# Optimization experiments

Measured on AMD Instinct MI355X. Metric: run time of the kernel, lower is better.

## Reference

```python
import jax, jax.numpy as jnp
import numpy as np

N_NODES = 50000
HIDDEN = 256
DEPTH = 6
NUM_GRAPHS = 500


def _build_graph(n):
    # 4-regular directed graph: node i -> (i+1, i-1, i+5, i-5) mod n.
    offs = np.array([1, -1, 5, -5], dtype=np.int64)
    src = np.repeat(np.arange(n, dtype=np.int64), 4)
    dst = (src + np.tile(offs, n)) % n
    # incoming edge ids of node u (edge id = 4*src + offset_index)
    u = np.arange(n, dtype=np.int64)
    incoming = np.stack([4 * ((u - 1) % n) + 0,
                         4 * ((u + 1) % n) + 1,
                         4 * ((u - 5) % n) + 2,
                         4 * ((u + 5) % n) + 3], axis=1)  # [n,4]
    E = 4 * n
    pred = incoming[src]           # [E,4] candidate line-graph predecessors of edge e
    pred_src = pred // 4           # source node of each predecessor edge
    keep = pred_src != dst[:, None]  # drop backtracking edge (exactly 1 per row)
    lg_src = pred[keep]                                   # [3E]
    lg_dst = np.repeat(np.arange(E, dtype=np.int64), 4)[keep.ravel()]  # [3E]
    return src, dst, lg_src, lg_dst


def setup_inputs() -> dict:
    key = jax.random.key(0)
    ks = jax.random.split(key, 8)
    n, H = N_NODES, HIDDEN
    E = 4 * n
    _, dst, lg_src, lg_dst = _build_graph(n)
    graph_ids = np.arange(n, dtype=np.int64) // (n // NUM_GRAPHS)
    s = 0.02  # small weight scale keeps relu message passing stable over DEPTH iters
    return {
        "x_nodes": jax.random.normal(ks[0], (n, 35), jnp.float32),
        "x_edges": jax.random.normal(ks[1], (E, 40), jnp.float32),
        "t_m": jax.random.normal(ks[2], (E, H), jnp.float32) * 0.1,
        "W_i": jax.random.normal(ks[3], (40, H), jnp.float32) * s,
        "W_h": jax.random.normal(ks[4], (H, H), jnp.float32) * s,
        "W_o": jax.random.normal(ks[5], (35 + H, H), jnp.float32) * s,
        "b_o": jax.random.normal(ks[6], (H,), jnp.float32) * s,
        "edge_dst": jnp.asarray(dst, jnp.int32),
        "lg_src": jnp.asarray(lg_src, jnp.int32),
        "lg_dst": jnp.asarray(lg_dst, jnp.int32),
        "graph_ids": jnp.asarray(graph_ids, jnp.int32),
        "num_graphs": NUM_GRAPHS,
    }


def reference(x_nodes, x_edges, t_m, W_i, W_h, W_o, b_o,
              edge_dst, lg_src, lg_dst, graph_ids, num_graphs):
    E = x_edges.shape[0]
    n = x_nodes.shape[0]
    binput = x_edges @ W_i                       # W_i has no bias
    g_m = jax.nn.relu(binput)                    # [E,H] per-edge message
    # tree-message aggregation over line graph is constant across depth iters
    t_agg = jax.ops.segment_sum(t_m[lg_src], lg_dst, num_segments=E)
    for _ in range(DEPTH - 1):
        g_agg = jax.ops.segment_sum(g_m[lg_src], lg_dst, num_segments=E)
        g_m = jax.nn.relu(binput + (g_agg + t_agg) @ W_h)
    # edge -> dst-node aggregation (copy_e + sum)
    nei1 = jax.ops.segment_sum(g_m, edge_dst, num_segments=n)
    nei2 = jax.ops.segment_sum(t_m, edge_dst, num_segments=n)
    ainput = jnp.concatenate([x_nodes, nei1 + nei2], axis=1)  # [n, 35+H]
    atom_hiddens = jax.nn.relu(ainput @ W_o + b_o)
    # dgl.mean_nodes: per-graph mean of node features
    sums = jax.ops.segment_sum(atom_hiddens, graph_ids, num_segments=num_graphs)
    counts = jax.ops.segment_sum(jnp.ones((n, 1), atom_hiddens.dtype), graph_ids,
                                 num_segments=num_graphs)
    return sums / counts
```

## Files before the change

kernel.cpp:

```cpp
#include <hip/hip_runtime.h>


#define H 256

typedef __attribute__((ext_vector_type(4))) float f32x4;
typedef __attribute__((ext_vector_type(8))) short bf16x8;

#define MFMA(a, b, c) __builtin_amdgcn_mfma_f32_16x16x32_bf16((a), (b), (c), 0, 0, 0)

__device__ __forceinline__ float bf2f(ushort u) {
  union { unsigned int i; float f; } v; v.i = ((unsigned int)u) << 16; return v.f;
}
__device__ __forceinline__ ushort f2bf(float f) {
  union { float f; unsigned int i; } v; v.f = f;
  unsigned int i = v.i;
  i += 0x7fffu + ((i >> 16) & 1u);
  return (ushort)(i >> 16);
}

union AFrag { bf16x8 v; ushort u[8]; };

__device__ __forceinline__ int edge_delta(int o) {
  return ((o & 2) ? 5 : 1) * ((o & 1) ? -1 : 1);
}

__device__ __forceinline__ int phi(int L) {
  return (L & ~31) | (((L >> 2) & 1) << 4) | (((L >> 3) & 3) << 2) | (L & 3);
}

__global__ __launch_bounds__(256) void prep_weights_kernel(
    const float* __restrict__ Wh, const float* __restrict__ Wi, const float* __restrict__ Wo,
    ushort* __restrict__ WhF, ushort* __restrict__ WiT,
    ushort* __restrict__ WoT1, ushort* __restrict__ WoT2) {
  const int nn = blockIdx.x;
  const int t = threadIdx.x;
  const int w = phi(nn);
  const int ch = w >> 7, nf = (w >> 4) & 7, l15 = w & 15;
  const int ks = t >> 5, kg = (t >> 3) & 3, i = t & 7;
  WhF[ch * 32768 + ((nf * 8 + ks) << 9) + (kg * 16 + l15) * 8 + i] = f2bf(Wh[t * H + nn]);
  WoT2[nn * H + t] = f2bf(Wo[(35 + t) * H + nn]);
  if (t < 64) {
    WiT[w * 64 + t] = (t < 40) ? f2bf(Wi[t * H + nn]) : (ushort)0;
    WoT1[nn * 64 + t] = (t < 35) ? f2bf(Wo[t * H + nn]) : (ushort)0;
  }
}

__global__ __launch_bounds__(256) void sum_tm_kernel(
    const float* __restrict__ t_m, ushort* __restrict__ t3, ushort* __restrict__ t4,
    int n, int useT4) {
  const int idx = blockIdx.x * 256 + threadIdx.x;
  const int s = idx >> 5;
  if (s >= n) return;
  const int cg = (idx & 31) * 8;
  int im1 = s - 1; if (im1 < 0) im1 += n;
  int ip1 = s + 1; if (ip1 >= n) ip1 -= n;
  int im5 = s - 5; if (im5 < 0) im5 += n;
  int ip5 = s + 5; if (ip5 >= n) ip5 -= n;
  const size_t e0 = (size_t)(4 * im1 + 0) * H + cg;
  const size_t e1 = (size_t)(4 * ip1 + 1) * H + cg;
  const size_t e2 = (size_t)(4 * im5 + 2) * H + cg;
  const size_t e3 = (size_t)(4 * ip5 + 3) * H + cg;
  f32x4 v0a = *(const f32x4*)(t_m + e0), v0b = *(const f32x4*)(t_m + e0 + 4);
  f32x4 v1a = *(const f32x4*)(t_m + e1), v1b = *(const f32x4*)(t_m + e1 + 4);
  f32x4 v2a = *(const f32x4*)(t_m + e2), v2b = *(const f32x4*)(t_m + e2 + 4);
  f32x4 v3a = *(const f32x4*)(t_m + e3), v3b = *(const f32x4*)(t_m + e3 + 4);
  f32x4 Sa = v0a + v1a + v2a + v3a;
  f32x4 Sb = v0b + v1b + v2b + v3b;
  f32x4 ra[4] = {Sa - v1a, Sa - v0a, Sa - v3a, Sa - v2a};
  f32x4 rb[4] = {Sb - v1b, Sb - v0b, Sb - v3b, Sb - v2b};
#pragma unroll
  for (int o = 0; o < 4; ++o) {
    AFrag a;
#pragma unroll
    for (int i = 0; i < 4; ++i) { a.u[i] = f2bf(ra[o][i]); a.u[4 + i] = f2bf(rb[o][i]); }
    *(bf16x8*)(t3 + (size_t)(4 * s + o) * H + cg) = a.v;
  }
  if (useT4) {
    AFrag a;
#pragma unroll
    for (int i = 0; i < 4; ++i) { a.u[i] = f2bf(Sa[i]); a.u[4 + i] = f2bf(Sb[i]); }
    *(bf16x8*)(t4 + (size_t)s * H + cg) = a.v;
  }
}

__global__ __launch_bounds__(512, 4) void prologue_kernel(
    const float* __restrict__ x_edges, const ushort* __restrict__ t3,
    const ushort* __restrict__ WhF, const ushort* __restrict__ WiT,
    ushort* __restrict__ tb, ushort* __restrict__ g0P, int E, int n) {
  extern __shared__ ushort lds[];
  const int tid = threadIdx.x;
  const int wid = tid >> 6, lane = tid & 63, l15 = lane & 15, kg = lane >> 4;
  const int ch = blockIdx.x >> 9;
  const int colbase = ch << 7;

  {
    const bf16x8* src = (const bf16x8*)(WhF + (size_t)colbase * H);
    bf16x8* dstl = (bf16x8*)lds;
#pragma unroll
    for (int j = 0; j < 8; ++j) dstl[tid + j * 512] = src[tid + j * 512];
  }
  __syncthreads();

  const int nchunks = (E + 127) >> 7;
  for (int c = blockIdx.x & 511; c < nchunks; c += 512) {
    const int row0 = (c << 7) + wid * 16;
    if (row0 >= E) continue;
    const int r = row0 + l15;

    const float* xp = x_edges + (size_t)r * 40;
    f32x4 xa0 = *(const f32x4*)(xp + kg * 8);
    f32x4 xa1 = *(const f32x4*)(xp + kg * 8 + 4);
    f32x4 xb0, xb1;
    if (kg == 0) { xb0 = *(const f32x4*)(xp + 32); xb1 = *(const f32x4*)(xp + 36); }

    bf16x8 av[8];
#pragma unroll
    for (int ks = 0; ks < 8; ++ks)
      av[ks] = *(const bf16x8*)(t3 + (size_t)r * H + ks * 32 + kg * 8);

    f32x4 acc[8];
#pragma unroll
    for (int i = 0; i < 8; ++i) acc[i] = (f32x4){0.f, 0.f, 0.f, 0.f};

    AFrag bx0, bx1;
#pragma unroll
    for (int i = 0; i < 4; ++i) { bx0.u[i] = f2bf(xa0[i]); bx0.u[4 + i] = f2bf(xa1[i]); }
    if (kg == 0) {
#pragma unroll
      for (int i = 0; i < 4; ++i) { bx1.u[i] = f2bf(xb0[i]); bx1.u[4 + i] = f2bf(xb1[i]); }
    } else {
#pragma unroll
      for (int i = 0; i < 8; ++i) bx1.u[i] = 0;
    }
#pragma unroll
    for (int nf = 0; nf < 8; ++nf) {
      const int w = colbase + nf * 16 + l15;
      bf16x8 a0 = *(const bf16x8*)(WiT + w * 64 + kg * 8);
      acc[nf] = MFMA(a0, bx0.v, acc[nf]);
      bf16x8 a1 = *(const bf16x8*)(WiT + w * 64 + 32 + kg * 8);
      acc[nf] = MFMA(a1, bx1.v, acc[nf]);
    }

    const int s_ = r >> 2, o_ = r & 3;
    int d_ = s_ + edge_delta(o_);
    if (d_ < 0) d_ += n; else if (d_ >= n) d_ -= n;
    ushort* gout = g0P + (size_t)(4 * d_ + o_) * H + colbase + kg * 8;
#pragma unroll
    for (int tt = 0; tt < 4; ++tt) {
      AFrag pk;
#pragma unroll
      for (int i = 0; i < 4; ++i) {
        pk.u[i]     = f2bf(fmaxf(acc[2 * tt][i], 0.f));
        pk.u[4 + i] = f2bf(fmaxf(acc[2 * tt + 1][i], 0.f));
      }
      *(bf16x8*)(gout + tt * 32) = pk.v;
    }

#pragma unroll
    for (int ks = 0; ks < 8; ++ks) {
#pragma unroll
      for (int nf = 0; nf < 8; ++nf) {
        bf16x8 a = *(const bf16x8*)(lds + ((nf * 8 + ks) << 9) + (lane << 3));
        acc[nf] = MFMA(a, av[ks], acc[nf]);
      }
    }

    ushort* tbp = tb + (size_t)r * H + colbase + kg * 8;
#pragma unroll
    for (int tt = 0; tt < 4; ++tt) {
      AFrag pk;
#pragma unroll
      for (int i = 0; i < 4; ++i) {
        pk.u[i]     = f2bf(acc[2 * tt][i]);
        pk.u[4 + i] = f2bf(acc[2 * tt + 1][i]);
      }
      *(bf16x8*)(tbp + tt * 32) = pk.v;
    }
  }
}

__global__ __launch_bounds__(512, 4) void mp_iter_kernel(
    const ushort* __restrict__ gOldP, const ushort* __restrict__ tb,
    const ushort* __restrict__ WhF, ushort* __restrict__ gNewP, int E, int n) {
  extern __shared__ ushort lds[];
  const int tid = threadIdx.x;
  const int wid = tid >> 6, lane = tid & 63, l15 = lane & 15, kg = lane >> 4;
  const int ch = blockIdx.x >> 9;
  const int colbase = ch << 7;

  {
    const bf16x8* src = (const bf16x8*)(WhF + (size_t)colbase * H);
    bf16x8* dstl = (bf16x8*)lds;
#pragma unroll
    for (int j = 0; j < 8; ++j) dstl[tid + j * 512] = src[tid + j * 512];
  }
  __syncthreads();

  const int nchunks = (E + 127) >> 7;
  for (int c = blockIdx.x & 511; c < nchunks; c += 512) {
    const int row0 = (c << 7) + wid * 16;
    if (row0 >= E) continue;
    const int r = row0 + l15;

    bf16x8 av[8];
#pragma unroll
    for (int ks = 0; ks < 8; ++ks)
      av[ks] = *(const bf16x8*)(gOldP + (size_t)r * H + ks * 32 + kg * 8);

    bf16x8 tbv[4];
    const ushort* tbp = tb + (size_t)r * H + colbase + kg * 8;
#pragma unroll
    for (int tt = 0; tt < 4; ++tt) tbv[tt] = *(const bf16x8*)(tbp + tt * 32);

    f32x4 acc[8];
#pragma unroll
    for (int i = 0; i < 8; ++i) acc[i] = (f32x4){0.f, 0.f, 0.f, 0.f};

#pragma unroll
    for (int ks = 0; ks < 8; ++ks) {
#pragma unroll
      for (int nf = 0; nf < 8; ++nf) {
        bf16x8 a = *(const bf16x8*)(lds + ((nf * 8 + ks) << 9) + (lane << 3));
        acc[nf] = MFMA(a, av[ks], acc[nf]);
      }
    }

    const int s = r >> 2, o = r & 3;
    int d = s + edge_delta(o);
    if (d < 0) d += n; else if (d >= n) d -= n;
    ushort* gout = gNewP + (size_t)(4 * d + o) * H + colbase + kg * 8;
#pragma unroll
    for (int tt = 0; tt < 4; ++tt) {
      AFrag pk;
#pragma unroll
      for (int i = 0; i < 4; ++i) {
        const float G0 = acc[2 * tt][i];
        const float G1 = acc[2 * tt + 1][i];
        const float t0 = G0 + __shfl_xor(G0, 2);
        const float S0 = t0 + __shfl_xor(t0, 1);
        const float t1 = G1 + __shfl_xor(G1, 2);
        const float S1 = t1 + __shfl_xor(t1, 1);
        const float d0 = __shfl_xor(G0, 1);
        const float d1 = __shfl_xor(G1, 1);
        const float v0 = bf2f((ushort)tbv[tt][i])     + (S0 - d0);
        const float v1 = bf2f((ushort)tbv[tt][4 + i]) + (S1 - d1);
        pk.u[i]     = f2bf(fmaxf(v0, 0.f));
        pk.u[4 + i] = f2bf(fmaxf(v1, 0.f));
      }
      *(bf16x8*)(gout + tt * 32) = pk.v;
    }
  }
}

__global__ __launch_bounds__(256) void readout_kernel(
    const float* __restrict__ x_nodes, const float* __restrict__ t_m,
    const ushort* __restrict__ gP, const ushort* __restrict__ t4,
    const float* __restrict__ b_o,
    const ushort* __restrict__ WoT1, const ushort* __restrict__ WoT2,
    float* __restrict__ out, int n, int npg, int useT4) {
  const int gidx = blockIdx.x;
  const int wid = threadIdx.x >> 6;
  const int lane = threadIdx.x & 63;
  const int l15 = lane & 15;
  const int kg = lane >> 4;
  const int u0 = gidx * npg;

  __shared__ float red[H];

  f32x4 acc[2][16];
#pragma unroll
  for (int m = 0; m < 2; ++m)
#pragma unroll
    for (int i = 0; i < 16; ++i) acc[m][i] = (f32x4){0.f, 0.f, 0.f, 0.f};

  int uu[2]; bool mv[2]; int inc[2][4];
#pragma unroll
  for (int m = 0; m < 2; ++m) {
    const int mf = wid * 2 + m;
    const int rl = mf * 16 + l15;
    mv[m] = rl < npg;
    const int u = u0 + rl;
    uu[m] = u;
    if (mv[m]) {
      inc[m][0] = 4 * ((u - 1 + n) % n);
      inc[m][1] = 4 * ((u + 1) % n) + 1;
      inc[m][2] = 4 * ((u - 5 + n) % n) + 2;
      inc[m][3] = 4 * ((u + 5) % n) + 3;
    } else {
      inc[m][0] = inc[m][1] = inc[m][2] = inc[m][3] = 0;
    }
  }

#pragma unroll
  for (int ks = 0; ks < 2; ++ks) {
    const int k = ks * 32 + kg * 8;
#pragma unroll
    for (int m = 0; m < 2; ++m) {
      AFrag a;
#pragma unroll
      for (int i = 0; i < 8; ++i) {
        const int kk = k + i;
        a.u[i] = (mv[m] && kk < 35) ? f2bf(x_nodes[(size_t)uu[m] * 35 + kk]) : (ushort)0;
      }
#pragma unroll
      for (int nf = 0; nf < 16; ++nf) {
        bf16x8 b = *(const bf16x8*)(WoT1 + (nf * 16 + l15) * 64 + k);
        acc[m][nf] = MFMA(a.v, b, acc[m][nf]);
      }
    }
  }

#pragma unroll
  for (int ks = 0; ks < 8; ++ks) {
    const int k = ks * 32 + kg * 8;
#pragma unroll
    for (int m = 0; m < 2; ++m) {
      AFrag a;
      if (mv[m]) {
        float s[8];
#pragma unroll
        for (int i = 0; i < 8; ++i) s[i] = 0.f;
        const int e4 = 4 * uu[m];
#pragma unroll
        for (int j = 0; j < 4; ++j) {
          bf16x8 gv = *(const bf16x8*)(gP + (size_t)(e4 + j) * H + k);
#pragma unroll
          for (int i = 0; i < 8; ++i) s[i] += bf2f((ushort)gv[i]);
        }
        if (useT4) {
          bf16x8 tv = *(const bf16x8*)(t4 + (size_t)uu[m] * H + k);
#pragma unroll
          for (int i = 0; i < 8; ++i) s[i] += bf2f((ushort)tv[i]);
        } else {
#pragma unroll
          for (int j = 0; j < 4; ++j) {
            const float* tp = t_m + (size_t)inc[m][j] * H + k;
            f32x4 t0 = *(const f32x4*)tp;
            f32x4 t1 = *(const f32x4*)(tp + 4);
#pragma unroll
            for (int i = 0; i < 4; ++i) { s[i] += t0[i]; s[4 + i] += t1[i]; }
          }
        }
#pragma unroll
        for (int i = 0; i < 8; ++i) a.u[i] = f2bf(s[i]);
      } else {
#pragma unroll
        for (int i = 0; i < 8; ++i) a.u[i] = 0;
      }
#pragma unroll
      for (int nf = 0; nf < 16; ++nf) {
        bf16x8 b = *(const bf16x8*)(WoT2 + (nf * 16 + l15) * H + k);
        acc[m][nf] = MFMA(a.v, b, acc[m][nf]);
      }
    }
  }

  red[threadIdx.x] = 0.f;
  __syncthreads();

#pragma unroll
  for (int nf = 0; nf < 16; ++nf) {
    const int col = nf * 16 + l15;
    const float bias = b_o[col];
    float cs = 0.f;
#pragma unroll
    for (int m = 0; m < 2; ++m) {
#pragma unroll
      for (int j = 0; j < 4; ++j) {
        const int rr = (wid * 2 + m) * 16 + kg * 4 + j;
        if (rr < npg) cs += fmaxf(acc[m][nf][j] + bias, 0.f);
      }
    }
    cs += __shfl_xor(cs, 16);
    cs += __shfl_xor(cs, 32);
    if (kg == 0) atomicAdd(&red[col], cs);
  }
  __syncthreads();
  out[(size_t)gidx * H + threadIdx.x] = red[threadIdx.x] * (1.0f / (float)npg);
}

extern "C" void kernel_launch(void* const* d_in, const int* in_sizes, int n_in,
                              void* d_out, int out_size, void* d_ws, size_t ws_size,
                              hipStream_t stream) {
  const float* x_nodes = (const float*)d_in[0];
  const float* x_edges = (const float*)d_in[1];
  const float* t_m     = (const float*)d_in[2];
  const float* W_i     = (const float*)d_in[3];
  const float* W_h     = (const float*)d_in[4];
  const float* W_o     = (const float*)d_in[5];
  const float* b_o     = (const float*)d_in[6];
  (void)n_in;

  const int n = in_sizes[0] / 35;
  const int E = in_sizes[1] / 40;
  const int num_graphs = out_size / H;
  const int npg = n / num_graphs;

  char* ws = (char*)d_ws;
  ushort* WhF  = (ushort*)(ws);
  ushort* WiT  = (ushort*)(ws + 131072);
  ushort* WoT1 = (ushort*)(ws + 164 * 1024);
  ushort* WoT2 = (ushort*)(ws + 200 * 1024);
  size_t off = 336 * 1024;
  const size_t gbytes = (size_t)E * H * 2;
  ushort* tb = (ushort*)(ws + off); off += gbytes;
  ushort* gA = (ushort*)(ws + off); off += gbytes;
  ushort* gB = (ushort*)(ws + off); off += gbytes;
  ushort* t3 = gB;
  const size_t t4bytes = (size_t)n * H * 2;
  const int useT4 = (ws_size >= off + t4bytes) ? 1 : 0;
  ushort* t4 = (ushort*)(ws + off);

  prep_weights_kernel<<<256, 256, 0, stream>>>(W_h, W_i, W_o, WhF, WiT, WoT1, WoT2);
  sum_tm_kernel<<<(n * 32 + 255) / 256, 256, 0, stream>>>(t_m, t3, t4, n, useT4);
  prologue_kernel<<<1024, 512, 65536, stream>>>(x_edges, t3, WhF, WiT, tb, gA, E, n);

  ushort* src = gA;
  ushort* dst = gB;
  for (int it = 0; it < 5; ++it) {
    mp_iter_kernel<<<1024, 512, 65536, stream>>>(src, tb, WhF, dst, E, n);
    ushort* tmp = src; src = dst; dst = tmp;
  }

  readout_kernel<<<num_graphs, 256, 0, stream>>>(x_nodes, t_m, src, t4, b_o, WoT1, WoT2,
                                                 (float*)d_out, n, npg, useT4);
}
```

Before: 706.1 us.

## Split output columns into four 64-wide chunks to halve LDS and registers per block

The prologue and message-passing kernels now cover 64 output columns per block instead of 128, using 2048 blocks and 32 KB of LDS with launch bounds raised to 8 blocks per CU. The weight prep layout is reindexed so each 64-column chunk is contiguous. The A-operand rows are streamed with a two-deep rolling prefetch rather than all eight fragments held in registers, cutting register pressure to raise occupancy. In exchange, every input row of g and t3 is read by four blocks instead of two, doubling global and L2 read traffic for the A operand.

After: 890.3 us. 26.1% more time.

```diff
diff --git a/kernel.cpp b/kernel.cpp
--- a/kernel.cpp
+++ b/kernel.cpp
@@ -35,9 +35,9 @@
   const int nn = blockIdx.x;
   const int t = threadIdx.x;
   const int w = phi(nn);
-  const int ch = w >> 7, nf = (w >> 4) & 7, l15 = w & 15;
+  const int nfg = w >> 4, l15w = w & 15;
   const int ks = t >> 5, kg = (t >> 3) & 3, i = t & 7;
-  WhF[ch * 32768 + ((nf * 8 + ks) << 9) + (kg * 16 + l15) * 8 + i] = f2bf(Wh[t * H + nn]);
+  WhF[((nfg * 8 + ks) << 9) + ((kg << 4) + l15w) * 8 + i] = f2bf(Wh[t * H + nn]);
   WoT2[nn * H + t] = f2bf(Wo[(35 + t) * H + nn]);
   if (t < 64) {
     WiT[w * 64 + t] = (t < 40) ? f2bf(Wi[t * H + nn]) : (ushort)0;
@@ -83,7 +83,7 @@
   }
 }
 
-__global__ __launch_bounds__(512, 4) void prologue_kernel(
+__global__ __launch_bounds__(512, 8) void prologue_kernel(
     const float* __restrict__ x_edges, const ushort* __restrict__ t3,
     const ushort* __restrict__ WhF, const ushort* __restrict__ WiT,
     ushort* __restrict__ tb, ushort* __restrict__ g0P, int E, int n) {
@@ -91,13 +91,13 @@
   const int tid = threadIdx.x;
   const int wid = tid >> 6, lane = tid & 63, l15 = lane & 15, kg = lane >> 4;
   const int ch = blockIdx.x >> 9;
-  const int colbase = ch << 7;
+  const int colbase = ch << 6;
 
   {
-    const bf16x8* src = (const bf16x8*)(WhF + (size_t)colbase * H);
+    const bf16x8* src = (const bf16x8*)(WhF) + ch * 2048;
     bf16x8* dstl = (bf16x8*)lds;
 #pragma unroll
-    for (int j = 0; j < 8; ++j) dstl[tid + j * 512] = src[tid + j * 512];
+    for (int j = 0; j < 4; ++j) dstl[tid + j * 512] = src[tid + j * 512];
   }
   __syncthreads();
 
@@ -112,15 +112,13 @@
     f32x4 xa1 = *(const f32x4*)(xp + kg * 8 + 4);
     f32x4 xb0, xb1;
     if (kg == 0) { xb0 = *(const f32x4*)(xp + 32); xb1 = *(const f32x4*)(xp + 36); }
-
-    bf16x8 av[8];
-#pragma unroll
-    for (int ks = 0; ks < 8; ++ks)
-      av[ks] = *(const bf16x8*)(t3 + (size_t)r * H + ks * 32 + kg * 8);
-
-    f32x4 acc[8];
-#pragma unroll
-    for (int i = 0; i < 8; ++i) acc[i] = (f32x4){0.f, 0.f, 0.f, 0.f};
+    const ushort* t3r = t3 + (size_t)r * H + kg * 8;
+    bf16x8 av0 = *(const bf16x8*)(t3r);
+    bf16x8 av1 = *(const bf16x8*)(t3r + 32);
+
+    f32x4 acc[4];
+#pragma unroll
+    for (int i = 0; i < 4; ++i) acc[i] = (f32x4){0.f, 0.f, 0.f, 0.f};
 
     AFrag bx0, bx1;
 #pragma unroll
@@ -133,7 +131,7 @@
       for (int i = 0; i < 8; ++i) bx1.u[i] = 0;
     }
 #pragma unroll
-    for (int nf = 0; nf < 8; ++nf) {
+    for (int nf = 0; nf < 4; ++nf) {
       const int w = colbase + nf * 16 + l15;
       bf16x8 a0 = *(const bf16x8*)(WiT + w * 64 + kg * 8);
       acc[nf] = MFMA(a0, bx0.v, acc[nf]);
@@ -146,7 +144,7 @@
     if (d_ < 0) d_ += n; else if (d_ >= n) d_ -= n;
     ushort* gout = g0P + (size_t)(4 * d_ + o_) * H + colbase + kg * 8;
 #pragma unroll
-    for (int tt = 0; tt < 4; ++tt) {
+    for (int tt = 0; tt < 2; ++tt) {
       AFrag pk;
 #pragma unroll
       for (int i = 0; i < 4; ++i) {
@@ -158,16 +156,19 @@
 
 #pragma unroll
     for (int ks = 0; ks < 8; ++ks) {
-#pragma unroll
-      for (int nf = 0; nf < 8; ++nf) {
+      bf16x8 av2;
+      if (ks < 6) av2 = *(const bf16x8*)(t3r + (ks + 2) * 32);
+#pragma unroll
+      for (int nf = 0; nf < 4; ++nf) {
         bf16x8 a = *(const bf16x8*)(lds + ((nf * 8 + ks) << 9) + (lane << 3));
-        acc[nf] = MFMA(a, av[ks], acc[nf]);
-      }
+        acc[nf] = MFMA(a, av0, acc[nf]);
+      }
+      av0 = av1; av1 = av2;
     }
 
     ushort* tbp = tb + (size_t)r * H + colbase + kg * 8;
 #pragma unroll
-    for (int tt = 0; tt < 4; ++tt) {
+    for (int tt = 0; tt < 2; ++tt) {
       AFrag pk;
 #pragma unroll
       for (int i = 0; i < 4; ++i) {
@@ -179,20 +180,20 @@
   }
 }
 
-__global__ __launch_bounds__(512, 4) void mp_iter_kernel(
+__global__ __launch_bounds__(512, 8) void mp_iter_kernel(
     const ushort* __restrict__ gOldP, const ushort* __restrict__ tb,
     const ushort* __restrict__ WhF, ushort* __restrict__ gNewP, int E, int n) {
   extern __shared__ ushort lds[];
   const int tid = threadIdx.x;
   const int wid = tid >> 6, lane = tid & 63, l15 = lane & 15, kg = lane >> 4;
   const int ch = blockIdx.x >> 9;
-  const int colbase = ch << 7;
+  const int colbase = ch << 6;
 
   {
-    const bf16x8* src = (const bf16x8*)(WhF + (size_t)colbase * H);
+    const bf16x8* src = (const bf16x8*)(WhF) + ch * 2048;
     bf16x8* dstl = (bf16x8*)lds;
 #pragma unroll
-    for (int j = 0; j < 8; ++j) dstl[tid + j * 512] = src[tid + j * 512];
+    for (int j = 0; j < 4; ++j) dstl[tid + j * 512] = src[tid + j * 512];
   }
   __syncthreads();
 
@@ -202,27 +203,29 @@
     if (row0 >= E) continue;
     const int r = row0 + l15;
 
-    bf16x8 av[8];
-#pragma unroll
-    for (int ks = 0; ks < 8; ++ks)
-      av[ks] = *(const bf16x8*)(gOldP + (size_t)r * H + ks * 32 + kg * 8);
-
-    bf16x8 tbv[4];
+    const ushort* gr = gOldP + (size_t)r * H + kg * 8;
+    bf16x8 av0 = *(const bf16x8*)(gr);
+    bf16x8 av1 = *(const bf16x8*)(gr + 32);
+
+    bf16x8 tbv[2];
     const ushort* tbp = tb + (size_t)r * H + colbase + kg * 8;
 #pragma unroll
-    for (int tt = 0; tt < 4; ++tt) tbv[tt] = *(const bf16x8*)(tbp + tt * 32);
-
-    f32x4 acc[8];
-#pragma unroll
-    for (int i = 0; i < 8; ++i) acc[i] = (f32x4){0.f, 0.f, 0.f, 0.f};
+    for (int tt = 0; tt < 2; ++tt) tbv[tt] = *(const bf16x8*)(tbp + tt * 32);
+
+    f32x4 acc[4];
+#pragma unroll
+    for (int i = 0; i < 4; ++i) acc[i] = (f32x4){0.f, 0.f, 0.f, 0.f};
 
 #pragma unroll
     for (int ks = 0; ks < 8; ++ks) {
-#pragma unroll
-      for (int nf = 0; nf < 8; ++nf) {
+      bf16x8 av2;
+      if (ks < 6) av2 = *(const bf16x8*)(gr + (ks + 2) * 32);
+#pragma unroll
+      for (int nf = 0; nf < 4; ++nf) {
         bf16x8 a = *(const bf16x8*)(lds + ((nf * 8 + ks) << 9) + (lane << 3));
-        acc[nf] = MFMA(a, av[ks], acc[nf]);
-      }
+        acc[nf] = MFMA(a, av0, acc[nf]);
+      }
+      av0 = av1; av1 = av2;
     }
 
     const int s = r >> 2, o = r & 3;
@@ -230,7 +233,7 @@
     if (d < 0) d += n; else if (d >= n) d -= n;
     ushort* gout = gNewP + (size_t)(4 * d + o) * H + colbase + kg * 8;
 #pragma unroll
-    for (int tt = 0; tt < 4; ++tt) {
+    for (int tt = 0; tt < 2; ++tt) {
       AFrag pk;
 #pragma unroll
       for (int i = 0; i < 4; ++i) {
@@ -413,12 +416,12 @@
 
   prep_weights_kernel<<<256, 256, 0, stream>>>(W_h, W_i, W_o, WhF, WiT, WoT1, WoT2);
   sum_tm_kernel<<<(n * 32 + 255) / 256, 256, 0, stream>>>(t_m, t3, t4, n, useT4);
-  prologue_kernel<<<1024, 512, 65536, stream>>>(x_edges, t3, WhF, WiT, tb, gA, E, n);
+  prologue_kernel<<<2048, 512, 32768, stream>>>(x_edges, t3, WhF, WiT, tb, gA, E, n);
 
   ushort* src = gA;
   ushort* dst = gB;
   for (int it = 0; it < 5; ++it) {
-    mp_iter_kernel<<<1024, 512, 65536, stream>>>(src, tb, WhF, dst, E, n);
+    mp_iter_kernel<<<2048, 512, 32768, stream>>>(src, tb, WhF, dst, E, n);
     ushort* tmp = src; src = dst; dst = tmp;
   }
 
```
